# Kernel optimization log

Hardware: AMD Instinct MI355X
Metric: run time of the kernel (lower is better)

Reference implementation:

```python
import jax
import jax.numpy as jnp
import numpy as np
from jax import lax

VOCAB = 35095 + 2   # embedding rows (padding_idx=0)
WORD_DIM = 300
SENT_LEN = 3000
B = 4


def setup_inputs() -> dict:
    key = jax.random.key(0)
    ks = jax.random.split(key, 20)
    x = jax.random.randint(ks[0], (B, SENT_LEN), 0, VOCAB)
    emb = (jax.random.normal(ks[1], (VOCAB, WORD_DIM), jnp.float32) * 0.1).at[0].set(0.0)  # padding_idx=0
    w1 = jax.random.normal(ks[2], (100, 1, 3), jnp.float32) * 0.05
    b1 = jax.random.normal(ks[3], (100,), jnp.float32) * 0.01
    w2 = jax.random.normal(ks[4], (100, 1, 4), jnp.float32) * 0.05
    b2 = jax.random.normal(ks[5], (100,), jnp.float32) * 0.01
    w3 = jax.random.normal(ks[6], (100, 1, 5), jnp.float32) * 0.05
    b3 = jax.random.normal(ks[7], (100,), jnp.float32) * 0.01
    fcw1 = jax.random.normal(ks[8], (34, 300), jnp.float32) * 0.05
    fcb1 = jnp.zeros((34,), jnp.float32)
    fcw2 = jax.random.normal(ks[9], (4, 300), jnp.float32) * 0.05
    fcb2 = jnp.zeros((4,), jnp.float32)
    fcw3 = jax.random.normal(ks[10], (3, 300), jnp.float32) * 0.05
    fcb3 = jnp.zeros((3,), jnp.float32)
    fcw4 = jax.random.normal(ks[11], (44, 300), jnp.float32) * 0.05
    fcb4 = jnp.zeros((44,), jnp.float32)
    fcw5 = jax.random.normal(ks[12], (5, 300), jnp.float32) * 0.05
    fcb5 = jnp.zeros((5,), jnp.float32)
    return dict(x=x, emb=emb, w1=w1, b1=b1, w2=w2, b2=b2, w3=w3, b3=b3,
                fcw1=fcw1, fcb1=fcb1, fcw2=fcw2, fcb2=fcb2, fcw3=fcw3, fcb3=fcb3,
                fcw4=fcw4, fcb4=fcb4, fcw5=fcw5, fcb5=fcb5)


def _conv_block(e, w, b):
    # e: [B, 1, L]; w: [F, 1, K]; valid conv -> relu -> global max over length
    y = lax.conv_general_dilated(e, w, window_strides=(1,), padding='VALID',
                                 dimension_numbers=('NCH', 'OIH', 'NCH'))
    y = jax.nn.relu(y + b[None, :, None])
    return jnp.max(y, axis=-1)  # [B, F]  (AdaptiveMaxPool1d(1); dropout is identity in eval)


def reference(x, emb, w1, b1, w2, b2, w3, b3,
              fcw1, fcb1, fcw2, fcb2, fcw3, fcb3, fcw4, fcb4, fcw5, fcb5):
    e = emb[x].reshape(x.shape[0], 1, WORD_DIM * SENT_LEN)  # [B,1,900000]
    feats = jnp.concatenate([_conv_block(e, w1, b1),
                             _conv_block(e, w2, b2),
                             _conv_block(e, w3, b3)], axis=1)  # [B,300]
    out_subsite = feats @ fcw1.T + fcb1
    out_laterality = feats @ fcw2.T + fcb2
    out_behavior = feats @ fcw3.T + fcb3
    out_histology = feats @ fcw4.T + fcb4
    out_grade = feats @ fcw5.T + fcb5
    return (out_subsite, out_laterality, out_behavior, out_histology, out_grade)
```

## Files before the change

### kernel.cpp

```cpp
#include <hip/hip_runtime.h>
#include <stdint.h>

#define L_SEQ   900000
#define N_WORDS 3000
#define WDIM    300
#define NB      4
#define NFPAD   320
#define NT      256
#define STRIP   2048
#define STEPS   128
#define NSTG    2064
#define NSTRIPS 440
#define L_MAIN  899968

typedef __attribute__((ext_vector_type(8))) short    bf16x8;
typedef __attribute__((ext_vector_type(4))) float    f32x4;
typedef __attribute__((ext_vector_type(4))) unsigned u32x4v;

__device__ __forceinline__ unsigned bf16rne(float v) {
    unsigned b = __float_as_uint(v);
    return (b + 0x7FFFu + ((b >> 16) & 1u)) >> 16;
}
__device__ __forceinline__ unsigned monokey(float v) {
    unsigned u = __float_as_uint(v);
    return u ^ (unsigned)(((int)u >> 31) | 0x80000000);
}
__device__ __forceinline__ unsigned cvt_pk_bf16(float a, float b) {
    unsigned r;
    asm("v_cvt_pk_bf16_f32 %0, %1, %2" : "=v"(r) : "v"(a), "v"(b));
    return r;
}

__global__ __launch_bounds__(NT)
void conv_mfma_kernel(
    const int*   __restrict__ x,
    const float* __restrict__ emb,
    const float* __restrict__ w1, const float* __restrict__ w2, const float* __restrict__ w3,
    unsigned*    __restrict__ maxkey)
{
    __shared__ __align__(16) unsigned buf[2 * NSTG];

    const int tid = threadIdx.x;
    const int b   = blockIdx.y;
    const int bx  = blockIdx.x;

    if (bx == NSTRIPS) {
        float* tE = (float*)buf;
        if (tid < 48) {
            int pos = L_MAIN + tid;
            float v = 0.f;
            if (pos < L_SEQ) {
                int wd = pos / WDIM;
                v = emb[x[b * N_WORDS + wd] * WDIM + (pos - wd * WDIM)];
            }
            tE[tid] = v;
        }
        __syncthreads();
        for (int f = tid; f < 300; f += NT) {
            int K; const float* wp;
            if (f < 100)      { K = 3; wp = w1 + f * 3; }
            else if (f < 200) { K = 4; wp = w2 + (f - 100) * 4; }
            else              { K = 5; wp = w3 + (f - 200) * 5; }
            float wk0 = wp[0], wk1 = wp[1], wk2 = (K > 2) ? wp[2] : 0.f;
            float wk3 = (K > 3) ? wp[3] : 0.f, wk4 = (K > 4) ? wp[4] : 0.f;
            float m = -1e30f;
            int tmax = L_SEQ - K;
            for (int t = L_MAIN; t <= tmax; ++t) {
                int o = t - L_MAIN;
                float y = wk0 * tE[o] + wk1 * tE[o + 1] + wk2 * tE[o + 2]
                        + wk3 * tE[o + 3] + wk4 * tE[o + 4];
                m = fmaxf(m, y);
            }
            atomicMax(&maxkey[b * NFPAD + f], monokey(m));
        }
        return;
    }

    const int strip0 = bx * STRIP;

    float vv[9];
    #pragma unroll
    for (int k = 0; k < 9; ++k) {
        int s = tid + k * NT;
        int pos = strip0 + s;
        float v = 0.f;
        if (s < NSTG && pos < L_SEQ) {
            int wd = pos / WDIM;
            v = emb[x[b * N_WORDS + wd] * WDIM + (pos - wd * WDIM)];
        }
        vv[k] = v;
    }

    unsigned short* sW = (unsigned short*)buf;
    #pragma unroll
    for (int k = 0; k < 10; ++k) {
        int idx = tid + k * NT;
        int f = idx >> 3, j = idx & 7;
        float wv = 0.f;
        if (f < 100)      { if (j < 3) wv = w1[f * 3 + j]; }
        else if (f < 200) { if (j < 4) wv = w2[(f - 100) * 4 + j]; }
        else if (f < 300) { if (j < 5) wv = w3[(f - 200) * 5 + j]; }
        unsigned rh = bf16rne(wv);
        float lo = wv - __uint_as_float(rh << 16);
        sW[idx]        = (unsigned short)rh;
        sW[2560 + idx] = (unsigned short)bf16rne(lo);
    }
    __syncthreads();

    const int lane = tid & 63;
    const int wid  = tid >> 6;
    const int col  = lane & 15;
    const int q    = lane >> 4;
    const int part = q & 1;
    bf16x8 aw0, aw1, aw2, aw3, aw4;
    {
        int f = (5 * wid) * 16 + col;
        const unsigned short* wbase = &sW[part * 2560 + f * 8];
        aw0 = *(const bf16x8*)(const void*)(wbase + 0 * 128);
        aw1 = *(const bf16x8*)(const void*)(wbase + 1 * 128);
        aw2 = *(const bf16x8*)(const void*)(wbase + 2 * 128);
        aw3 = *(const bf16x8*)(const void*)(wbase + 3 * 128);
        aw4 = *(const bf16x8*)(const void*)(wbase + 4 * 128);
    }
    __syncthreads();

    float* rawE = (float*)buf;
    #pragma unroll
    for (int k = 0; k < 9; ++k) {
        int s = tid + k * NT;
        if (s < NSTG) rawE[s] = vv[k];
    }
    __syncthreads();
    float nv[9];
    #pragma unroll
    for (int k = 0; k < 9; ++k) {
        int s = tid + k * NT;
        nv[k] = (s + 1 < NSTG) ? rawE[s + 1] : 0.f;
    }
    __syncthreads();
    #pragma unroll
    for (int k = 0; k < 9; ++k) {
        int s = tid + k * NT;
        if (s < NSTG) {
            float v0 = vv[k], v1 = nv[k];
            unsigned u0 = __float_as_uint(v0), u1 = __float_as_uint(v1);
            float l0 = v0 - __uint_as_float(u0 & 0xFFFF0000u);
            float l1 = v1 - __uint_as_float(u1 & 0xFFFF0000u);
            buf[s]        = __builtin_amdgcn_perm(u1, u0, 0x07060302u);
            buf[NSTG + s] = cvt_pk_bf16(l0, l1);
        }
    }
    __syncthreads();

    int nsteps = (L_MAIN - strip0) / 16;
    if (nsteps > STEPS) nsteps = STEPS;

    const f32x4 Z = {0.f, 0.f, 0.f, 0.f};
    f32x4 rm0 = {-1e30f,-1e30f,-1e30f,-1e30f}, rm1 = rm0, rm2 = rm0, rm3 = rm0, rm4 = rm0;

    const unsigned* bp = buf + ((lane >> 5) ? NSTG : 0) + col;
    for (int s = 0; s < nsteps; s += 2) {
        u32x4v ba = {bp[0],  bp[2],  bp[4],  bp[6]};
        u32x4v bb = {bp[16], bp[18], bp[20], bp[22]};
        bf16x8 Bav = __builtin_bit_cast(bf16x8, ba);
        bf16x8 Bbv = __builtin_bit_cast(bf16x8, bb);
        f32x4 d0 = __builtin_amdgcn_mfma_f32_16x16x32_bf16(aw0, Bav, Z, 0, 0, 0);
        f32x4 d1 = __builtin_amdgcn_mfma_f32_16x16x32_bf16(aw1, Bav, Z, 0, 0, 0);
        f32x4 d2 = __builtin_amdgcn_mfma_f32_16x16x32_bf16(aw2, Bav, Z, 0, 0, 0);
        f32x4 d3 = __builtin_amdgcn_mfma_f32_16x16x32_bf16(aw3, Bav, Z, 0, 0, 0);
        f32x4 d4 = __builtin_amdgcn_mfma_f32_16x16x32_bf16(aw4, Bav, Z, 0, 0, 0);
        #pragma unroll
        for (int r = 0; r < 4; ++r) {
            rm0[r] = fmaxf(rm0[r], d0[r]);
            rm1[r] = fmaxf(rm1[r], d1[r]);
            rm2[r] = fmaxf(rm2[r], d2[r]);
            rm3[r] = fmaxf(rm3[r], d3[r]);
            rm4[r] = fmaxf(rm4[r], d4[r]);
        }
        d0 = __builtin_amdgcn_mfma_f32_16x16x32_bf16(aw0, Bbv, Z, 0, 0, 0);
        d1 = __builtin_amdgcn_mfma_f32_16x16x32_bf16(aw1, Bbv, Z, 0, 0, 0);
        d2 = __builtin_amdgcn_mfma_f32_16x16x32_bf16(aw2, Bbv, Z, 0, 0, 0);
        d3 = __builtin_amdgcn_mfma_f32_16x16x32_bf16(aw3, Bbv, Z, 0, 0, 0);
        d4 = __builtin_amdgcn_mfma_f32_16x16x32_bf16(aw4, Bbv, Z, 0, 0, 0);
        #pragma unroll
        for (int r = 0; r < 4; ++r) {
            rm0[r] = fmaxf(rm0[r], d0[r]);
            rm1[r] = fmaxf(rm1[r], d1[r]);
            rm2[r] = fmaxf(rm2[r], d2[r]);
            rm3[r] = fmaxf(rm3[r], d3[r]);
            rm4[r] = fmaxf(rm4[r], d4[r]);
        }
        bp += 32;
    }

    f32x4 rms[5] = {rm0, rm1, rm2, rm3, rm4};
    #pragma unroll
    for (int t = 0; t < 5; ++t) {
        #pragma unroll
        for (int r = 0; r < 4; ++r) {
            float v = rms[t][r];
            v = fmaxf(v, __shfl_xor(v, 1));
            v = fmaxf(v, __shfl_xor(v, 2));
            v = fmaxf(v, __shfl_xor(v, 4));
            v = fmaxf(v, __shfl_xor(v, 8));
            if (col == 0) {
                int f = (5 * wid + t) * 16 + q * 4 + r;
                atomicMax(&maxkey[b * NFPAD + f], monokey(v));
            }
        }
    }
}

__global__ __launch_bounds__(128) void fc_kernel(
    const unsigned* __restrict__ maxkey,
    const float* __restrict__ cb1, const float* __restrict__ cb2, const float* __restrict__ cb3,
    const float* __restrict__ fw1, const float* __restrict__ fb1,
    const float* __restrict__ fw2, const float* __restrict__ fb2,
    const float* __restrict__ fw3, const float* __restrict__ fb3,
    const float* __restrict__ fw4, const float* __restrict__ fb4,
    const float* __restrict__ fw5, const float* __restrict__ fb5,
    float* __restrict__ out)
{
    __shared__ __align__(16) float feats[WDIM];
    const int b   = blockIdx.x;
    const int tid = threadIdx.x;

    for (int f = tid; f < WDIM; f += 128) {
        unsigned k = maxkey[b * NFPAD + f];
        unsigned u = (k & 0x80000000u) ? (k ^ 0x80000000u) : ~k;
        float y = __uint_as_float(u);
        float bias = (f < 100) ? cb1[f] : (f < 200) ? cb2[f - 100] : cb3[f - 200];
        feats[f] = fmaxf(0.f, y + bias);
    }
    __syncthreads();

    if (tid >= 90) return;
    const float* Wh; const float* Bh; int dim, off, j;
    int n = tid;
    if      (n < 34) { Wh = fw1; Bh = fb1; dim = 34; off = 0;   j = n;      }
    else if (n < 38) { Wh = fw2; Bh = fb2; dim = 4;  off = 136; j = n - 34; }
    else if (n < 41) { Wh = fw3; Bh = fb3; dim = 3;  off = 152; j = n - 38; }
    else if (n < 85) { Wh = fw4; Bh = fb4; dim = 44; off = 164; j = n - 41; }
    else             { Wh = fw5; Bh = fb5; dim = 5;  off = 340; j = n - 85; }

    float acc = Bh[j];
    const float* wr = Wh + j * WDIM;
    #pragma unroll 5
    for (int k = 0; k < WDIM; k += 4) {
        float4 wv = *reinterpret_cast<const float4*>(wr + k);
        acc = fmaf(wv.x, feats[k + 0], acc);
        acc = fmaf(wv.y, feats[k + 1], acc);
        acc = fmaf(wv.z, feats[k + 2], acc);
        acc = fmaf(wv.w, feats[k + 3], acc);
    }
    out[off + b * dim + j] = acc;
}

extern "C" void kernel_launch(void* const* d_in, const int* in_sizes, int n_in,
                              void* d_out, int out_size, void* d_ws, size_t ws_size,
                              hipStream_t stream) {
    const int*   x    = (const int*)  d_in[0];
    const float* emb  = (const float*)d_in[1];
    const float* w1   = (const float*)d_in[2];
    const float* b1   = (const float*)d_in[3];
    const float* w2   = (const float*)d_in[4];
    const float* b2   = (const float*)d_in[5];
    const float* w3   = (const float*)d_in[6];
    const float* b3   = (const float*)d_in[7];
    const float* fw1  = (const float*)d_in[8];
    const float* fb1  = (const float*)d_in[9];
    const float* fw2  = (const float*)d_in[10];
    const float* fb2  = (const float*)d_in[11];
    const float* fw3  = (const float*)d_in[12];
    const float* fb3  = (const float*)d_in[13];
    const float* fw4  = (const float*)d_in[14];
    const float* fb4  = (const float*)d_in[15];
    const float* fw5  = (const float*)d_in[16];
    const float* fb5  = (const float*)d_in[17];
    float*    out    = (float*)d_out;
    unsigned* maxkey = (unsigned*)d_ws;

    hipMemsetAsync(maxkey, 0, NB * NFPAD * sizeof(unsigned), stream);

    dim3 grid(NSTRIPS + 1, NB);
    conv_mfma_kernel<<<grid, NT, 0, stream>>>(x, emb, w1, w2, w3, maxkey);

    fc_kernel<<<NB, 128, 0, stream>>>(maxkey, b1, b2, b3,
                                      fw1, fb1, fw2, fb2, fw3, fb3,
                                      fw4, fb4, fw5, fb5, out);
}
```

Baseline: 230.6 us.

## Split embedding gather and bf16 packing into a separate pre-pass kernel

Adds a pack kernel that gathers embeddings, splits them into hi/lo bf16 pairs in global workspace, pre-splits the conv weights, and zeroes the max buffer, which replaces the memset. The conv kernel now drops its LDS staging and barriers and reads the packed operands straight from global memory, with a one-iteration register prefetch. This trades the per-block LDS staging and sync cost for an extra kernel launch and a round trip of about 29 MB through global memory, and the strided 4-byte global loads may be slower than LDS reads.

After: 256.5 us. +11.2%, slower.

```diff
diff --git a/kernel.cpp b/kernel.cpp
--- a/kernel.cpp
+++ b/kernel.cpp
@@ -9,9 +9,9 @@
 #define NT      256
 #define STRIP   2048
 #define STEPS   128
-#define NSTG    2064
 #define NSTRIPS 440
 #define L_MAIN  899968
+#define NPP     900016
 
 typedef __attribute__((ext_vector_type(8))) short    bf16x8;
 typedef __attribute__((ext_vector_type(4))) float    f32x4;
@@ -31,30 +31,70 @@
     return r;
 }
 
-__global__ __launch_bounds__(NT)
-void conv_mfma_kernel(
+__device__ __forceinline__ float gatherE(const int* __restrict__ x,
+                                         const float* __restrict__ emb,
+                                         int b, int pos) {
+    if (pos >= L_SEQ) return 0.f;
+    int wd = pos / WDIM;
+    int d  = pos - wd * WDIM;
+    return emb[x[b * N_WORDS + wd] * WDIM + d];
+}
+
+__global__ __launch_bounds__(NT) void pack_kernel(
     const int*   __restrict__ x,
     const float* __restrict__ emb,
     const float* __restrict__ w1, const float* __restrict__ w2, const float* __restrict__ w3,
+    unsigned*       __restrict__ uEhi,
+    unsigned*       __restrict__ uElo,
+    unsigned short* __restrict__ wsplit,
+    unsigned*       __restrict__ maxkey)
+{
+    const int tid = threadIdx.x;
+    const int b   = blockIdx.y;
+    const int p   = blockIdx.x * NT + tid;
+
+    if (p < NPP) {
+        float v0 = gatherE(x, emb, b, p);
+        float v1 = gatherE(x, emb, b, p + 1);
+        unsigned u0 = __float_as_uint(v0), u1 = __float_as_uint(v1);
+        float l0 = v0 - __uint_as_float(u0 & 0xFFFF0000u);
+        float l1 = v1 - __uint_as_float(u1 & 0xFFFF0000u);
+        uEhi[b * NPP + p] = __builtin_amdgcn_perm(u1, u0, 0x07060302u);
+        uElo[b * NPP + p] = cvt_pk_bf16(l0, l1);
+    }
+
+    if (blockIdx.y == 0 && blockIdx.x < 10) {
+        int widx = blockIdx.x * NT + tid;
+        int f = widx >> 3, j = widx & 7;
+        float wv = 0.f;
+        if (f < 100)      { if (j < 3) wv = w1[f * 3 + j]; }
+        else if (f < 200) { if (j < 4) wv = w2[(f - 100) * 4 + j]; }
+        else if (f < 300) { if (j < 5) wv = w3[(f - 200) * 5 + j]; }
+        unsigned rh = bf16rne(wv);
+        float lo = wv - __uint_as_float(rh << 16);
+        wsplit[widx]        = (unsigned short)rh;
+        wsplit[2560 + widx] = (unsigned short)bf16rne(lo);
+        if (widx < NB * NFPAD) maxkey[widx] = 0u;
+    }
+}
+
+__global__ __launch_bounds__(NT) void conv_mfma_kernel(
+    const int*   __restrict__ x,
+    const float* __restrict__ emb,
+    const float* __restrict__ w1, const float* __restrict__ w2, const float* __restrict__ w3,
+    const unsigned*       __restrict__ uEhi,
+    const unsigned*       __restrict__ uElo,
+    const unsigned short* __restrict__ wsplit,
     unsigned*    __restrict__ maxkey)
 {
-    __shared__ __align__(16) unsigned buf[2 * NSTG];
+    __shared__ float tE[48];
 
     const int tid = threadIdx.x;
     const int b   = blockIdx.y;
     const int bx  = blockIdx.x;
 
     if (bx == NSTRIPS) {
-        float* tE = (float*)buf;
-        if (tid < 48) {
-            int pos = L_MAIN + tid;
-            float v = 0.f;
-            if (pos < L_SEQ) {
-                int wd = pos / WDIM;
-                v = emb[x[b * N_WORDS + wd] * WDIM + (pos - wd * WDIM)];
-            }
-            tE[tid] = v;
-        }
+        if (tid < 48) tE[tid] = gatherE(x, emb, b, L_MAIN + tid);
         __syncthreads();
         for (int f = tid; f < 300; f += NT) {
             int K; const float* wp;
@@ -77,80 +117,18 @@
     }
 
     const int strip0 = bx * STRIP;
-
-    float vv[9];
-    #pragma unroll
-    for (int k = 0; k < 9; ++k) {
-        int s = tid + k * NT;
-        int pos = strip0 + s;
-        float v = 0.f;
-        if (s < NSTG && pos < L_SEQ) {
-            int wd = pos / WDIM;
-            v = emb[x[b * N_WORDS + wd] * WDIM + (pos - wd * WDIM)];
-        }
-        vv[k] = v;
-    }
-
-    unsigned short* sW = (unsigned short*)buf;
-    #pragma unroll
-    for (int k = 0; k < 10; ++k) {
-        int idx = tid + k * NT;
-        int f = idx >> 3, j = idx & 7;
-        float wv = 0.f;
-        if (f < 100)      { if (j < 3) wv = w1[f * 3 + j]; }
-        else if (f < 200) { if (j < 4) wv = w2[(f - 100) * 4 + j]; }
-        else if (f < 300) { if (j < 5) wv = w3[(f - 200) * 5 + j]; }
-        unsigned rh = bf16rne(wv);
-        float lo = wv - __uint_as_float(rh << 16);
-        sW[idx]        = (unsigned short)rh;
-        sW[2560 + idx] = (unsigned short)bf16rne(lo);
-    }
-    __syncthreads();
-
     const int lane = tid & 63;
     const int wid  = tid >> 6;
     const int col  = lane & 15;
     const int q    = lane >> 4;
     const int part = q & 1;
-    bf16x8 aw0, aw1, aw2, aw3, aw4;
-    {
-        int f = (5 * wid) * 16 + col;
-        const unsigned short* wbase = &sW[part * 2560 + f * 8];
-        aw0 = *(const bf16x8*)(const void*)(wbase + 0 * 128);
-        aw1 = *(const bf16x8*)(const void*)(wbase + 1 * 128);
-        aw2 = *(const bf16x8*)(const void*)(wbase + 2 * 128);
-        aw3 = *(const bf16x8*)(const void*)(wbase + 3 * 128);
-        aw4 = *(const bf16x8*)(const void*)(wbase + 4 * 128);
-    }
-    __syncthreads();
-
-    float* rawE = (float*)buf;
-    #pragma unroll
-    for (int k = 0; k < 9; ++k) {
-        int s = tid + k * NT;
-        if (s < NSTG) rawE[s] = vv[k];
-    }
-    __syncthreads();
-    float nv[9];
-    #pragma unroll
-    for (int k = 0; k < 9; ++k) {
-        int s = tid + k * NT;
-        nv[k] = (s + 1 < NSTG) ? rawE[s + 1] : 0.f;
-    }
-    __syncthreads();
-    #pragma unroll
-    for (int k = 0; k < 9; ++k) {
-        int s = tid + k * NT;
-        if (s < NSTG) {
-            float v0 = vv[k], v1 = nv[k];
-            unsigned u0 = __float_as_uint(v0), u1 = __float_as_uint(v1);
-            float l0 = v0 - __uint_as_float(u0 & 0xFFFF0000u);
-            float l1 = v1 - __uint_as_float(u1 & 0xFFFF0000u);
-            buf[s]        = __builtin_amdgcn_perm(u1, u0, 0x07060302u);
-            buf[NSTG + s] = cvt_pk_bf16(l0, l1);
-        }
-    }
-    __syncthreads();
+
+    const unsigned short* wb = wsplit + part * 2560 + ((5 * wid) * 16 + col) * 8;
+    bf16x8 aw0 = *(const bf16x8*)(const void*)(wb + 0 * 128);
+    bf16x8 aw1 = *(const bf16x8*)(const void*)(wb + 1 * 128);
+    bf16x8 aw2 = *(const bf16x8*)(const void*)(wb + 2 * 128);
+    bf16x8 aw3 = *(const bf16x8*)(const void*)(wb + 3 * 128);
+    bf16x8 aw4 = *(const bf16x8*)(const void*)(wb + 4 * 128);
 
     int nsteps = (L_MAIN - strip0) / 16;
     if (nsteps > STEPS) nsteps = STEPS;
@@ -158,10 +136,13 @@
     const f32x4 Z = {0.f, 0.f, 0.f, 0.f};
     f32x4 rm0 = {-1e30f,-1e30f,-1e30f,-1e30f}, rm1 = rm0, rm2 = rm0, rm3 = rm0, rm4 = rm0;
 
-    const unsigned* bp = buf + ((lane >> 5) ? NSTG : 0) + col;
+    const unsigned* bp = ((lane >> 5) ? uElo : uEhi) + b * NPP + strip0 + col;
+
+    u32x4v ba = {bp[0],  bp[2],  bp[4],  bp[6]};
+    u32x4v bb = {bp[16], bp[18], bp[20], bp[22]};
     for (int s = 0; s < nsteps; s += 2) {
-        u32x4v ba = {bp[0],  bp[2],  bp[4],  bp[6]};
-        u32x4v bb = {bp[16], bp[18], bp[20], bp[22]};
+        u32x4v na = {bp[32], bp[34], bp[36], bp[38]};
+        u32x4v nb = {bp[48], bp[50], bp[52], bp[54]};
         bf16x8 Bav = __builtin_bit_cast(bf16x8, ba);
         bf16x8 Bbv = __builtin_bit_cast(bf16x8, bb);
         f32x4 d0 = __builtin_amdgcn_mfma_f32_16x16x32_bf16(aw0, Bav, Z, 0, 0, 0);
@@ -190,6 +171,7 @@
             rm3[r] = fmaxf(rm3[r], d3[r]);
             rm4[r] = fmaxf(rm4[r], d4[r]);
         }
+        ba = na; bb = nb;
         bp += 32;
     }
 
@@ -277,13 +259,20 @@
     const float* fb4  = (const float*)d_in[15];
     const float* fw5  = (const float*)d_in[16];
     const float* fb5  = (const float*)d_in[17];
-    float*    out    = (float*)d_out;
-    unsigned* maxkey = (unsigned*)d_ws;
-
-    hipMemsetAsync(maxkey, 0, NB * NFPAD * sizeof(unsigned), stream);
-
-    dim3 grid(NSTRIPS + 1, NB);
-    conv_mfma_kernel<<<grid, NT, 0, stream>>>(x, emb, w1, w2, w3, maxkey);
+    float* out = (float*)d_out;
+
+    unsigned*       maxkey = (unsigned*)d_ws;
+    unsigned*       uEhi   = maxkey + NB * NFPAD;
+    unsigned*       uElo   = uEhi + NB * NPP;
+    unsigned short* wsplit = (unsigned short*)(uElo + NB * NPP);
+
+    dim3 pgrid((NPP + NT - 1) / NT, NB);
+    pack_kernel<<<pgrid, NT, 0, stream>>>(x, emb, w1, w2, w3,
+                                          uEhi, uElo, wsplit, maxkey);
+
+    dim3 cgrid(NSTRIPS + 1, NB);
+    conv_mfma_kernel<<<cgrid, NT, 0, stream>>>(x, emb, w1, w2, w3,
+                                               uEhi, uElo, wsplit, maxkey);
 
     fc_kernel<<<NB, 128, 0, stream>>>(maxkey, b1, b2, b3,
                                       fw1, fb1, fw2, fb2, fw3, fb3,
```
